# Performance work log

Measured on AMD Instinct MI355X. Metric: run time of the kernel, lower is better.

Reference implementation:

```python
import jax, jax.numpy as jnp
import numpy as np
from jax import lax

DIM = 192
HEADS = 4

def setup_inputs() -> dict:
    key = jax.random.key(0)
    k1, k2, k3, k4 = jax.random.split(key, 4)
    x = jax.random.normal(k1, (8, DIM, 128, 128), dtype=jnp.float32)
    w_qkv = jax.random.normal(k2, (DIM * 3, DIM), dtype=jnp.float32) * 0.05
    w_dw = jax.random.normal(k3, (DIM * 3, 1, 3, 3), dtype=jnp.float32) * 0.1
    w_proj = jax.random.normal(k4, (DIM, DIM), dtype=jnp.float32) * 0.05
    temperature = jnp.ones((HEADS, 1, 1), dtype=jnp.float32)
    return {"x": x, "w_qkv": w_qkv, "w_dw": w_dw, "w_proj": w_proj, "temperature": temperature}

def _l2norm(t, eps=1e-12):
    # F.normalize(t, dim=-1): t / max(||t||_2, eps)
    n = jnp.sqrt(jnp.sum(t * t, axis=-1, keepdims=True))
    return t / jnp.maximum(n, eps)

def reference(x, w_qkv, w_dw, w_proj, temperature):
    b, c, h, w = x.shape
    heads = temperature.shape[0]
    ch = c // heads  # channels per head
    # 1x1 conv (pointwise): dim -> 3*dim
    qkv = jnp.einsum('oi,bihw->bohw', w_qkv, x)
    # 3x3 depthwise conv, groups = 3*dim, padding 1
    qkv = lax.conv_general_dilated(
        qkv, w_dw, window_strides=(1, 1), padding='SAME',
        dimension_numbers=('NCHW', 'OIHW', 'NCHW'),
        feature_group_count=3 * c)
    q, k, v = jnp.split(qkv, 3, axis=1)
    # b (head c) h w -> b head c (h w)
    q = q.reshape(b, heads, ch, h * w)
    k = k.reshape(b, heads, ch, h * w)
    v = v.reshape(b, heads, ch, h * w)
    qn = _l2norm(q)
    kn = _l2norm(k)
    # channel-channel attention: [b, head, ch, ch]
    attn = jnp.einsum('bhcn,bhdn->bhcd', qn, kn) * temperature[None]
    attn = jax.nn.relu(attn)
    out = jnp.einsum('bhcd,bhdn->bhcn', attn, v)
    out = out.reshape(b, c, h, w)
    # output 1x1 projection
    out = jnp.einsum('oi,bihw->bohw', w_proj, out)
    return out
```

## Files before the change

### kernel.cpp

```cpp
#include <hip/hip_runtime.h>

#define BB 8
#define CC 192
#define C3 576
#define HW 16384
#define HEADS 4
#define CHD 48
#define NPLANE (BB*CC)

typedef short s8v __attribute__((ext_vector_type(8)));
typedef float f16v __attribute__((ext_vector_type(16)));
typedef float f4v __attribute__((ext_vector_type(4)));

__device__ __forceinline__ ushort bfu(float f) {
    union { float f; unsigned u; } c; c.f = f;
    unsigned u = c.u + 0x7FFFu + ((c.u >> 16) & 1u);
    return (ushort)(u >> 16);
}
__device__ __forceinline__ float ubf(ushort u) {
    union { unsigned u; float f; } c; c.u = ((unsigned)u) << 16;
    return c.f;
}

__global__ void kw_cvt(const float* __restrict__ w, ushort* __restrict__ wbf) {
    int idx = blockIdx.x * 256 + threadIdx.x;
    if (idx >= C3 * CC) return;
    int o = idx / CC, k = idx % CC;
    int sec = o / CC;
    int ol = o - sec * CC;
    wbf[(size_t)sec * CC * CC + (size_t)(k >> 3) * CC * 8 + ol * 8 + (k & 7)] = bfu(w[idx]);
}

template<int SRC>
__global__ __launch_bounds__(256) void k_trans(
    const float* __restrict__ xf, const ushort* __restrict__ xh,
    ushort* __restrict__ T)
{
    const int b = blockIdx.x, cg = blockIdx.y;
    const int p = blockIdx.z * 1024 + threadIdx.x * 4;
    float a[8][4];
    #pragma unroll
    for (int c = 0; c < 8; c++) {
        if (SRC == 0) {
            *(float4*)a[c] = *(const float4*)(xf + ((size_t)(b * CC + cg * 8 + c) * HW + p));
        } else {
            ushort4 u = *(const ushort4*)(xh + ((size_t)(b * CC + cg * 8 + c) * HW + p));
            a[c][0] = ubf(u.x); a[c][1] = ubf(u.y); a[c][2] = ubf(u.z); a[c][3] = ubf(u.w);
        }
    }
    #pragma unroll
    for (int j = 0; j < 4; j++) {
        unsigned wp[4];
        #pragma unroll
        for (int i = 0; i < 4; i++)
            wp[i] = (unsigned)bfu(a[2*i][j]) | ((unsigned)bfu(a[2*i+1][j]) << 16);
        *(uint4*)(T + ((size_t)(b * 24 + cg) * HW + p + j) * 8) = *(const uint4*)wp;
    }
}

template<int MODE>
__global__ __launch_bounds__(256) void gemm_mfma(
    const ushort* __restrict__ A,
    const ushort* __restrict__ BT,
    ushort* __restrict__ qk, ushort* __restrict__ vpl,
    float* __restrict__ outf)
{
    __shared__ ushort Rep[MODE == 0 ? 192 * 136 : 8];
    int lin = blockIdx.x, sec, pt, b;
    if (MODE == 0) {
        int logical = (lin & 7) * 384 + (lin >> 3);
        sec = logical % 3;
        int pb = logical / 3;
        pt = pb & 127; b = pb >> 7;
    } else {
        int logical = (lin & 7) * 128 + (lin >> 3);
        sec = 0; b = logical >> 7; pt = logical & 127;
    }
    const int t = threadIdx.x, lane = t & 63, w = t >> 6;
    const int wr = w >> 1, wc = w & 1;
    const int ll = lane & 31, kg = lane >> 5;
    const int pbase = pt * 128;
    const ushort* Ab = A + (size_t)(MODE == 0 ? sec : b) * CC * CC;
    const ushort* Bb = BT + (size_t)b * 24 * HW * 8;

    f16v acc[3][2];
    #pragma unroll
    for (int mt = 0; mt < 3; mt++)
        #pragma unroll
        for (int nt = 0; nt < 2; nt++)
            #pragma unroll
            for (int i = 0; i < 16; i++) acc[mt][nt][i] = 0.f;

    #pragma unroll 4
    for (int ks = 0; ks < 12; ks++) {
        s8v af[3], bfr[2];
        #pragma unroll
        for (int mt = 0; mt < 3; mt++)
            af[mt] = *(const s8v*)(Ab + ((size_t)(ks * 2 + kg) * CC + wr * 96 + mt * 32 + ll) * 8);
        #pragma unroll
        for (int nt = 0; nt < 2; nt++)
            bfr[nt] = *(const s8v*)(Bb + ((size_t)(ks * 2 + kg) * HW + pbase + wc * 64 + nt * 32 + ll) * 8);
        #pragma unroll
        for (int mt = 0; mt < 3; mt++)
            #pragma unroll
            for (int nt = 0; nt < 2; nt++)
                acc[mt][nt] = __builtin_amdgcn_mfma_f32_32x32x16_bf16(af[mt], bfr[nt], acc[mt][nt], 0, 0, 0);
    }

    if (MODE == 0) {
        #pragma unroll
        for (int mt = 0; mt < 3; mt++)
            #pragma unroll
            for (int nt = 0; nt < 2; nt++)
                #pragma unroll
                for (int g = 0; g < 4; g++)
                    #pragma unroll
                    for (int j = 0; j < 4; j++)
                        Rep[(wr * 96 + mt * 32 + 8 * g + 4 * kg + j) * 136
                            + wc * 64 + nt * 32 + ll] = bfu(acc[mt][nt][4 * g + j]);
        __syncthreads();
        ushort* ob = (sec == 2) ? vpl + (size_t)b * CC * HW
                                : qk + (size_t)(sec * BB + b) * CC * HW;
        #pragma unroll
        for (int i = 0; i < 12; i++) {
            int idx = i * 256 + t;
            int row = idx >> 4, c8 = idx & 15;
            int4 vv = *(const int4*)&Rep[row * 136 + c8 * 8];
            *(int4*)(ob + (size_t)row * HW + pbase + c8 * 8) = vv;
        }
    } else {
        #pragma unroll
        for (int mt = 0; mt < 3; mt++)
            #pragma unroll
            for (int nt = 0; nt < 2; nt++)
                #pragma unroll
                for (int r = 0; r < 16; r++) {
                    int o = wr * 96 + mt * 32 + (r & 3) + 8 * (r >> 2) + 4 * kg;
                    int p = pbase + wc * 64 + nt * 32 + ll;
                    outf[((size_t)b * CC + o) * HW + p] = acc[mt][nt][r];
                }
    }
}

__global__ __launch_bounds__(256) void k_dw_bf(
    ushort* __restrict__ qk, ushort* __restrict__ vb,
    const float* __restrict__ wdw, float* __restrict__ sq, float* __restrict__ sk)
{
    __shared__ ushort rows[10][128];
    __shared__ float red[4];
    int pid = blockIdx.x;
    int sec = pid / NPLANE, rem = pid % NPLANE;
    int b = rem / CC, c = rem % CC;
    ushort* p = sec < 2 ? qk + ((size_t)(sec * BB + b) * CC + c) * HW
                        : vb + ((size_t)b * CC + c) * HW;
    const float* wc9 = wdw + (size_t)(sec * CC + c) * 9;
    float w0=wc9[0],w1=wc9[1],w2=wc9[2],w3=wc9[3],w4=wc9[4],w5=wc9[5],w6=wc9[6],w7=wc9[7],w8=wc9[8];
    const int t = threadIdx.x, lr = t >> 5, lx = (t & 31) * 4;
    float ss = 0.f;
    if (t < 32) ((ushort4*)rows[0])[t] = ((const ushort4*)p)[t];
    __syncthreads();
    for (int y0 = 0; y0 < 128; y0 += 8) {
        int ry = y0 + 1 + lr;
        if (ry < 128) *(ushort4*)&rows[ry % 10][lx] = *(const ushort4*)(p + (size_t)ry * 128 + lx);
        __syncthreads();
        const int oy = y0 + lr;
        float a0=0,a1=0,a2=0,a3=0;
        if (oy >= 1) {
            const ushort* rw = rows[(oy - 1) % 10];
            float m0=ubf(rw[lx]),m1=ubf(rw[lx+1]),m2=ubf(rw[lx+2]),m3=ubf(rw[lx+3]);
            float lf = lx ? ubf(rw[lx-1]) : 0.f, rt = (lx < 124) ? ubf(rw[lx+4]) : 0.f;
            a0 += w0*lf + w1*m0 + w2*m1;  a1 += w0*m0 + w1*m1 + w2*m2;
            a2 += w0*m1 + w1*m2 + w2*m3;  a3 += w0*m2 + w1*m3 + w2*rt;
        }
        {
            const ushort* rw = rows[oy % 10];
            float m0=ubf(rw[lx]),m1=ubf(rw[lx+1]),m2=ubf(rw[lx+2]),m3=ubf(rw[lx+3]);
            float lf = lx ? ubf(rw[lx-1]) : 0.f, rt = (lx < 124) ? ubf(rw[lx+4]) : 0.f;
            a0 += w3*lf + w4*m0 + w5*m1;  a1 += w3*m0 + w4*m1 + w5*m2;
            a2 += w3*m1 + w4*m2 + w5*m3;  a3 += w3*m2 + w4*m3 + w5*rt;
        }
        if (oy + 1 < 128) {
            const ushort* rw = rows[(oy + 1) % 10];
            float m0=ubf(rw[lx]),m1=ubf(rw[lx+1]),m2=ubf(rw[lx+2]),m3=ubf(rw[lx+3]);
            float lf = lx ? ubf(rw[lx-1]) : 0.f, rt = (lx < 124) ? ubf(rw[lx+4]) : 0.f;
            a0 += w6*lf + w7*m0 + w8*m1;  a1 += w6*m0 + w7*m1 + w8*m2;
            a2 += w6*m1 + w7*m2 + w8*m3;  a3 += w6*m2 + w7*m3 + w8*rt;
        }
        ss += a0*a0 + a1*a1 + a2*a2 + a3*a3;
        __syncthreads();
        ushort4 o4; o4.x = bfu(a0); o4.y = bfu(a1); o4.z = bfu(a2); o4.w = bfu(a3);
        *(ushort4*)(p + (size_t)oy * 128 + lx) = o4;
    }
    if (sec < 2) {
        for (int off = 32; off; off >>= 1) ss += __shfl_down(ss, off);
        if ((t & 63) == 0) red[t >> 6] = ss;
        __syncthreads();
        if (t == 0) (sec == 0 ? sq : sk)[b * CC + c] = red[0] + red[1] + red[2] + red[3];
    }
}

__global__ __launch_bounds__(256) void k_gram(
    const ushort* __restrict__ qk, float* __restrict__ G)
{
    int slab = blockIdx.x, h = blockIdx.y, b = blockIdx.z;
    const int t = threadIdx.x, lane = t & 63, w = t >> 6;
    const ushort* qb = qk + ((size_t)b * CC + h * CHD) * HW;
    const ushort* kb = qk + ((size_t)(BB + b) * CC + h * CHD) * HW;
    const int ll = lane & 15, lh = lane >> 4;
    f4v acc[3][3];
    #pragma unroll
    for (int i = 0; i < 3; i++)
        #pragma unroll
        for (int j = 0; j < 3; j++)
            #pragma unroll
            for (int r = 0; r < 4; r++) acc[i][j][r] = 0.f;
    const int nbase = slab * 1024 + w * 256 + lh * 8;
    for (int s = 0; s < 8; s++) {
        const int n = nbase + s * 32;
        s8v aq[3], bk[3];
        #pragma unroll
        for (int mt = 0; mt < 3; mt++)
            aq[mt] = *(const s8v*)(qb + (size_t)(mt * 16 + ll) * HW + n);
        #pragma unroll
        for (int mt = 0; mt < 3; mt++)
            bk[mt] = *(const s8v*)(kb + (size_t)(mt * 16 + ll) * HW + n);
        #pragma unroll
        for (int i = 0; i < 3; i++)
            #pragma unroll
            for (int j = 0; j < 3; j++)
                acc[i][j] = __builtin_amdgcn_mfma_f32_16x16x32_bf16(aq[i], bk[j], acc[i][j], 0, 0, 0);
    }
    float* Gb = G + (size_t)(b * HEADS + h) * CHD * CHD;
    #pragma unroll
    for (int i = 0; i < 3; i++)
        #pragma unroll
        for (int j = 0; j < 3; j++)
            #pragma unroll
            for (int r = 0; r < 4; r++) {
                int c = i * 16 + lh * 4 + r, d = j * 16 + ll;
                atomicAdd(&Gb[c * CHD + d], acc[i][j][r]);
            }
}

__global__ __launch_bounds__(256) void k_compose(
    const float* __restrict__ G, const float* __restrict__ sq, const float* __restrict__ sk,
    const float* __restrict__ temp, const float* __restrict__ wproj,
    ushort* __restrict__ Mbf)
{
    __shared__ float attnS[CHD * CHD];
    __shared__ float wS[CC * CHD];
    int h = blockIdx.x, b = blockIdx.y, t = threadIdx.x;
    float tv = temp[h];
    const float* Gb = G + (size_t)(b * HEADS + h) * CHD * CHD;
    const float* sqb = sq + b * CC + h * CHD;
    const float* skb = sk + b * CC + h * CHD;
    #pragma unroll
    for (int i = 0; i < 9; i++) {
        int idx = i * 256 + t;
        int c = idx / CHD, d = idx % CHD;
        float nq = fmaxf(sqrtf(sqb[c]), 1e-12f);
        float nk = fmaxf(sqrtf(skb[d]), 1e-12f);
        float v = Gb[idx] * tv / (nq * nk);
        attnS[idx] = fmaxf(v, 0.f);
    }
    #pragma unroll
    for (int i = 0; i < 36; i++) {
        int idx = i * 256 + t;
        wS[idx] = wproj[(idx / CHD) * CC + h * CHD + idx % CHD];
    }
    __syncthreads();
    ushort* Mb = Mbf + (size_t)b * CC * CC;
    #pragma unroll
    for (int i = 0; i < 36; i++) {
        int idx = i * 256 + t;
        int o = idx / CHD, d = idx % CHD;
        float s = 0.f;
        #pragma unroll 8
        for (int c2 = 0; c2 < CHD; c2++)
            s += wS[o * CHD + c2] * attnS[c2 * CHD + d];
        int cglob = h * CHD + d;
        Mb[(size_t)(cglob >> 3) * CC * 8 + o * 8 + (cglob & 7)] = bfu(s);
    }
}

extern "C" void kernel_launch(void* const* d_in, const int* in_sizes, int n_in,
                              void* d_out, int out_size, void* d_ws, size_t ws_size,
                              hipStream_t stream)
{
    const float* x      = (const float*)d_in[0];
    const float* w_qkv  = (const float*)d_in[1];
    const float* w_dw   = (const float*)d_in[2];
    const float* w_proj = (const float*)d_in[3];
    const float* temp   = (const float*)d_in[4];
    float* out = (float*)d_out;

    ushort* qk = (ushort*)d_out;

    ushort* xT = (ushort*)d_ws;
    ushort* vb = xT + (size_t)BB * CC * HW;
    float*  G  = (float*)(vb + (size_t)BB * CC * HW);
    float*  sq = G + (size_t)BB * HEADS * CHD * CHD;
    float*  sk = sq + (size_t)BB * CC;
    ushort* wbf = (ushort*)(sk + (size_t)BB * CC);
    ushort* Mbf = wbf + (size_t)C3 * CC;

    kw_cvt<<<dim3((C3 * CC + 255) / 256), 256, 0, stream>>>(w_qkv, wbf);
    hipMemsetAsync(G, 0, (size_t)BB * HEADS * CHD * CHD * sizeof(float), stream);

    k_trans<0><<<dim3(BB, 24, 16), 256, 0, stream>>>(x, nullptr, xT);

    gemm_mfma<0><<<dim3(3072), 256, 0, stream>>>(wbf, xT, qk, vb, nullptr);

    k_dw_bf<<<dim3(3 * NPLANE), 256, 0, stream>>>(qk, vb, w_dw, sq, sk);

    k_trans<1><<<dim3(BB, 24, 16), 256, 0, stream>>>(nullptr, vb, xT);

    k_gram<<<dim3(16, HEADS, BB), 256, 0, stream>>>(qk, G);

    k_compose<<<dim3(HEADS, BB), 256, 0, stream>>>(G, sq, sk, temp, w_proj, Mbf);

    gemm_mfma<1><<<dim3(1024), 256, 0, stream>>>(Mbf, xT, nullptr, nullptr, out);
}
```

Before: 401.2 us.

## Fuse V depthwise conv with transpose, double-buffer GEMM loads, direct stores, split gram

A new kernel runs the V-section depthwise conv and writes the result straight into the channel-interleaved transposed layout. This removes the separate in-place V pass and the second transpose kernel. The QKV GEMM now double-buffers its fragment loads across k-steps and writes bf16 outputs directly from registers instead of staging them through LDS. The gram kernel uses twice as many slabs, each half as large. The direct scattered 2-byte global stores may coalesce worse than the old LDS-staged 16-byte stores, and the extra gram slabs double the number of atomic adds.

Result: no change. 398.4 us (-0.7%).

```diff
diff --git a/kernel.cpp b/kernel.cpp
--- a/kernel.cpp
+++ b/kernel.cpp
@@ -31,23 +31,15 @@
     wbf[(size_t)sec * CC * CC + (size_t)(k >> 3) * CC * 8 + ol * 8 + (k & 7)] = bfu(w[idx]);
 }
 
-template<int SRC>
 __global__ __launch_bounds__(256) void k_trans(
-    const float* __restrict__ xf, const ushort* __restrict__ xh,
-    ushort* __restrict__ T)
+    const float* __restrict__ xf, ushort* __restrict__ T)
 {
     const int b = blockIdx.x, cg = blockIdx.y;
     const int p = blockIdx.z * 1024 + threadIdx.x * 4;
     float a[8][4];
     #pragma unroll
-    for (int c = 0; c < 8; c++) {
-        if (SRC == 0) {
-            *(float4*)a[c] = *(const float4*)(xf + ((size_t)(b * CC + cg * 8 + c) * HW + p));
-        } else {
-            ushort4 u = *(const ushort4*)(xh + ((size_t)(b * CC + cg * 8 + c) * HW + p));
-            a[c][0] = ubf(u.x); a[c][1] = ubf(u.y); a[c][2] = ubf(u.z); a[c][3] = ubf(u.w);
-        }
-    }
+    for (int c = 0; c < 8; c++)
+        *(float4*)a[c] = *(const float4*)(xf + ((size_t)(b * CC + cg * 8 + c) * HW + p));
     #pragma unroll
     for (int j = 0; j < 4; j++) {
         unsigned wp[4];
@@ -56,6 +48,17 @@
             wp[i] = (unsigned)bfu(a[2*i][j]) | ((unsigned)bfu(a[2*i+1][j]) << 16);
         *(uint4*)(T + ((size_t)(b * 24 + cg) * HW + p + j) * 8) = *(const uint4*)wp;
     }
+}
+
+__device__ __forceinline__ void loadk(int ks, const ushort* Ab, const ushort* Bb,
+    int kg, int wr, int wc, int ll, int pbase, s8v a[3], s8v b[2])
+{
+    #pragma unroll
+    for (int mt = 0; mt < 3; mt++)
+        a[mt] = *(const s8v*)(Ab + ((size_t)(ks * 2 + kg) * CC + wr * 96 + mt * 32 + ll) * 8);
+    #pragma unroll
+    for (int nt = 0; nt < 2; nt++)
+        b[nt] = *(const s8v*)(Bb + ((size_t)(ks * 2 + kg) * HW + pbase + wc * 64 + nt * 32 + ll) * 8);
 }
 
 template<int MODE>
@@ -65,7 +68,6 @@
     ushort* __restrict__ qk, ushort* __restrict__ vpl,
     float* __restrict__ outf)
 {
-    __shared__ ushort Rep[MODE == 0 ? 192 * 136 : 8];
     int lin = blockIdx.x, sec, pt, b;
     if (MODE == 0) {
         int logical = (lin & 7) * 384 + (lin >> 3);
@@ -91,43 +93,37 @@
             #pragma unroll
             for (int i = 0; i < 16; i++) acc[mt][nt][i] = 0.f;
 
-    #pragma unroll 4
-    for (int ks = 0; ks < 12; ks++) {
-        s8v af[3], bfr[2];
-        #pragma unroll
-        for (int mt = 0; mt < 3; mt++)
-            af[mt] = *(const s8v*)(Ab + ((size_t)(ks * 2 + kg) * CC + wr * 96 + mt * 32 + ll) * 8);
-        #pragma unroll
-        for (int nt = 0; nt < 2; nt++)
-            bfr[nt] = *(const s8v*)(Bb + ((size_t)(ks * 2 + kg) * HW + pbase + wc * 64 + nt * 32 + ll) * 8);
+    s8v a0[3], b0[2], a1[3], b1[2];
+    loadk(0, Ab, Bb, kg, wr, wc, ll, pbase, a0, b0);
+    #pragma unroll
+    for (int kk = 0; kk < 6; kk++) {
+        loadk(2 * kk + 1, Ab, Bb, kg, wr, wc, ll, pbase, a1, b1);
         #pragma unroll
         for (int mt = 0; mt < 3; mt++)
             #pragma unroll
             for (int nt = 0; nt < 2; nt++)
-                acc[mt][nt] = __builtin_amdgcn_mfma_f32_32x32x16_bf16(af[mt], bfr[nt], acc[mt][nt], 0, 0, 0);
+                acc[mt][nt] = __builtin_amdgcn_mfma_f32_32x32x16_bf16(a0[mt], b0[nt], acc[mt][nt], 0, 0, 0);
+        if (kk < 5) loadk(2 * kk + 2, Ab, Bb, kg, wr, wc, ll, pbase, a0, b0);
+        #pragma unroll
+        for (int mt = 0; mt < 3; mt++)
+            #pragma unroll
+            for (int nt = 0; nt < 2; nt++)
+                acc[mt][nt] = __builtin_amdgcn_mfma_f32_32x32x16_bf16(a1[mt], b1[nt], acc[mt][nt], 0, 0, 0);
     }
 
     if (MODE == 0) {
+        ushort* ob = (sec == 2) ? vpl + (size_t)b * CC * HW
+                                : qk + (size_t)(sec * BB + b) * CC * HW;
         #pragma unroll
         for (int mt = 0; mt < 3; mt++)
             #pragma unroll
             for (int nt = 0; nt < 2; nt++)
                 #pragma unroll
-                for (int g = 0; g < 4; g++)
-                    #pragma unroll
-                    for (int j = 0; j < 4; j++)
-                        Rep[(wr * 96 + mt * 32 + 8 * g + 4 * kg + j) * 136
-                            + wc * 64 + nt * 32 + ll] = bfu(acc[mt][nt][4 * g + j]);
-        __syncthreads();
-        ushort* ob = (sec == 2) ? vpl + (size_t)b * CC * HW
-                                : qk + (size_t)(sec * BB + b) * CC * HW;
-        #pragma unroll
-        for (int i = 0; i < 12; i++) {
-            int idx = i * 256 + t;
-            int row = idx >> 4, c8 = idx & 15;
-            int4 vv = *(const int4*)&Rep[row * 136 + c8 * 8];
-            *(int4*)(ob + (size_t)row * HW + pbase + c8 * 8) = vv;
-        }
+                for (int r = 0; r < 16; r++) {
+                    int o = wr * 96 + mt * 32 + (r & 3) + 8 * (r >> 2) + 4 * kg;
+                    int p = pbase + wc * 64 + nt * 32 + ll;
+                    ob[(size_t)o * HW + p] = bfu(acc[mt][nt][r]);
+                }
     } else {
         #pragma unroll
         for (int mt = 0; mt < 3; mt++)
@@ -143,7 +139,7 @@
 }
 
 __global__ __launch_bounds__(256) void k_dw_bf(
-    ushort* __restrict__ qk, ushort* __restrict__ vb,
+    ushort* __restrict__ qk,
     const float* __restrict__ wdw, float* __restrict__ sq, float* __restrict__ sk)
 {
     __shared__ ushort rows[10][128];
@@ -151,8 +147,7 @@
     int pid = blockIdx.x;
     int sec = pid / NPLANE, rem = pid % NPLANE;
     int b = rem / CC, c = rem % CC;
-    ushort* p = sec < 2 ? qk + ((size_t)(sec * BB + b) * CC + c) * HW
-                        : vb + ((size_t)b * CC + c) * HW;
+    ushort* p = qk + ((size_t)(sec * BB + b) * CC + c) * HW;
     const float* wc9 = wdw + (size_t)(sec * CC + c) * 9;
     float w0=wc9[0],w1=wc9[1],w2=wc9[2],w3=wc9[3],w4=wc9[4],w5=wc9[5],w6=wc9[6],w7=wc9[7],w8=wc9[8];
     const int t = threadIdx.x, lr = t >> 5, lx = (t & 31) * 4;
@@ -191,11 +186,75 @@
         ushort4 o4; o4.x = bfu(a0); o4.y = bfu(a1); o4.z = bfu(a2); o4.w = bfu(a3);
         *(ushort4*)(p + (size_t)oy * 128 + lx) = o4;
     }
-    if (sec < 2) {
-        for (int off = 32; off; off >>= 1) ss += __shfl_down(ss, off);
-        if ((t & 63) == 0) red[t >> 6] = ss;
+    for (int off = 32; off; off >>= 1) ss += __shfl_down(ss, off);
+    if ((t & 63) == 0) red[t >> 6] = ss;
+    __syncthreads();
+    if (t == 0) (sec == 0 ? sq : sk)[b * CC + c] = red[0] + red[1] + red[2] + red[3];
+}
+
+__global__ __launch_bounds__(256) void k_dw_v(
+    const ushort* __restrict__ vb, const float* __restrict__ wdw,
+    ushort* __restrict__ vT)
+{
+    __shared__ ushort obuf[4][8][128];
+    const int cg = blockIdx.x, b = blockIdx.y, yq = blockIdx.z;
+    const int t = threadIdx.x;
+    const int c = t >> 5, lr = (t >> 3) & 3, xo = t & 7;
+    const int ch = cg * 8 + c;
+    const ushort* p = vb + ((size_t)b * CC + ch) * HW;
+    const float* wc9 = wdw + (size_t)(2 * CC + ch) * 9;
+    float wt[9];
+    #pragma unroll
+    for (int i = 0; i < 9; i++) wt[i] = wc9[i];
+    ushort* tb = vT + (size_t)(b * 24 + cg) * HW * 8;
+    const int x0 = xo * 16;
+
+    for (int ic = 0; ic < 8; ic++) {
+        const int y = yq * 32 + ic * 4 + lr;
+        float a[16];
+        #pragma unroll
+        for (int j = 0; j < 16; j++) a[j] = 0.f;
+        #pragma unroll
+        for (int dy = 0; dy < 3; dy++) {
+            int ry = y - 1 + dy;
+            if (ry >= 0 && ry < 128) {
+                const ushort* r = p + (size_t)ry * 128 + x0;
+                float wv[18];
+                uint4 v0 = *(const uint4*)r;
+                uint4 v1 = *(const uint4*)(r + 8);
+                unsigned uu[8] = {v0.x, v0.y, v0.z, v0.w, v1.x, v1.y, v1.z, v1.w};
+                #pragma unroll
+                for (int q = 0; q < 8; q++) {
+                    union { unsigned u; float f; } lo, hi;
+                    lo.u = uu[q] << 16;  hi.u = uu[q] & 0xFFFF0000u;
+                    wv[1 + 2*q] = lo.f;  wv[2 + 2*q] = hi.f;
+                }
+                wv[0]  = x0 ? ubf(r[-1]) : 0.f;
+                wv[17] = (x0 < 112) ? ubf(r[16]) : 0.f;
+                float t0 = wt[dy*3], t1 = wt[dy*3+1], t2 = wt[dy*3+2];
+                #pragma unroll
+                for (int j = 0; j < 16; j++)
+                    a[j] += t0 * wv[j] + t1 * wv[j+1] + t2 * wv[j+2];
+            }
+        }
         __syncthreads();
-        if (t == 0) (sec == 0 ? sq : sk)[b * CC + c] = red[0] + red[1] + red[2] + red[3];
+        ushort tmp[16];
+        #pragma unroll
+        for (int j = 0; j < 16; j++) tmp[j] = bfu(a[j]);
+        *(int4*)&obuf[lr][c][x0]     = *(int4*)&tmp[0];
+        *(int4*)&obuf[lr][c][x0 + 8] = *(int4*)&tmp[8];
+        __syncthreads();
+        #pragma unroll
+        for (int rep = 0; rep < 2; rep++) {
+            int u = t + rep * 256;
+            int row = u >> 7, x = u & 127;
+            int4 gi;
+            ushort* g = (ushort*)&gi;
+            #pragma unroll
+            for (int cc = 0; cc < 8; cc++) g[cc] = obuf[row][cc][x];
+            int yg = yq * 32 + ic * 4 + row;
+            *(int4*)(tb + ((size_t)yg * 128 + x) * 8) = gi;
+        }
     }
 }
 
@@ -214,8 +273,9 @@
         for (int j = 0; j < 3; j++)
             #pragma unroll
             for (int r = 0; r < 4; r++) acc[i][j][r] = 0.f;
-    const int nbase = slab * 1024 + w * 256 + lh * 8;
-    for (int s = 0; s < 8; s++) {
+    const int nbase = slab * 512 + w * 128 + lh * 8;
+    #pragma unroll
+    for (int s = 0; s < 4; s++) {
         const int n = nbase + s * 32;
         s8v aq[3], bk[3];
         #pragma unroll
@@ -237,8 +297,8 @@
         for (int j = 0; j < 3; j++)
             #pragma unroll
             for (int r = 0; r < 4; r++) {
-                int c = i * 16 + lh * 4 + r, d = j * 16 + ll;
-                atomicAdd(&Gb[c * CHD + d], acc[i][j][r]);
+                int cc = i * 16 + lh * 4 + r, d = j * 16 + ll;
+                atomicAdd(&Gb[cc * CHD + d], acc[i][j][r]);
             }
 }
 
@@ -307,15 +367,15 @@
     kw_cvt<<<dim3((C3 * CC + 255) / 256), 256, 0, stream>>>(w_qkv, wbf);
     hipMemsetAsync(G, 0, (size_t)BB * HEADS * CHD * CHD * sizeof(float), stream);
 
-    k_trans<0><<<dim3(BB, 24, 16), 256, 0, stream>>>(x, nullptr, xT);
+    k_trans<<<dim3(BB, 24, 16), 256, 0, stream>>>(x, xT);
 
     gemm_mfma<0><<<dim3(3072), 256, 0, stream>>>(wbf, xT, qk, vb, nullptr);
 
-    k_dw_bf<<<dim3(3 * NPLANE), 256, 0, stream>>>(qk, vb, w_dw, sq, sk);
-
-    k_trans<1><<<dim3(BB, 24, 16), 256, 0, stream>>>(nullptr, vb, xT);
-
-    k_gram<<<dim3(16, HEADS, BB), 256, 0, stream>>>(qk, G);
+    k_dw_bf<<<dim3(2 * NPLANE), 256, 0, stream>>>(qk, w_dw, sq, sk);
+
+    k_dw_v<<<dim3(24, BB, 4), 256, 0, stream>>>(vb, w_dw, xT);
+
+    k_gram<<<dim3(32, HEADS, BB), 256, 0, stream>>>(qk, G);
 
     k_compose<<<dim3(HEADS, BB), 256, 0, stream>>>(G, sq, sk, temp, w_proj, Mbf);
 
```
